# Kernel optimization log

Measured on AMD Instinct MI355X. Metric: run time of the kernel, lower is better.

Reference implementation:

```python
import jax, jax.numpy as jnp
import numpy as np

EPS = 1e-8

def _layernorm(x, gamma, beta):
    # torch-style: std with Bessel correction (ddof=1), eps added to std
    D = x.shape[-1]
    mean = jnp.mean(x, axis=-1, keepdims=True)
    var = jnp.sum((x - mean) ** 2, axis=-1, keepdims=True) / (D - 1)
    std = jnp.sqrt(var)
    return (x - mean) / (std + EPS) * gamma + beta


def setup_inputs() -> dict:
    key = jax.random.key(0)
    B, T, D, H = 1, 2048, 1024, 16
    Dh = D // H
    ks = jax.random.split(key, 8)
    s = 0.02
    return {
        "x": jax.random.normal(ks[0], (B, T, D), jnp.float32),
        "wq": jax.random.normal(ks[1], (H, D, Dh), jnp.float32) * s,
        "wk": jax.random.normal(ks[2], (H, D, Dh), jnp.float32) * s,
        "wv": jax.random.normal(ks[3], (H, D, Dh), jnp.float32) * s,
        "wo": jax.random.normal(ks[4], (D, D), jnp.float32) * s,
        "bo": jnp.zeros((D,), jnp.float32),
        "ln1_g": jnp.ones((D,), jnp.float32),
        "ln1_b": jnp.zeros((D,), jnp.float32),
        "ln2_g": jnp.ones((D,), jnp.float32),
        "ln2_b": jnp.zeros((D,), jnp.float32),
        "w1": jax.random.normal(ks[5], (D, 4 * D), jnp.float32) * s,
        "b1": jnp.zeros((4 * D,), jnp.float32),
        "w2": jax.random.normal(ks[6], (4 * D, D), jnp.float32) * s,
        "b2": jnp.zeros((D,), jnp.float32),
    }


def reference(x, wq, wk, wv, wo, bo, ln1_g, ln1_b, ln2_g, ln2_b, w1, b1, w2, b2):
    B, T, D = x.shape
    H, _, Dh = wq.shape
    # --- attention sublayer (dropout p used at eval => identity) ---
    h = _layernorm(x, ln1_g, ln1_b)
    q = jnp.einsum('btd,hde->bhte', h, wq)
    k = jnp.einsum('btd,hde->bhte', h, wk)
    v = jnp.einsum('btd,hde->bhte', h, wv)
    scores = jnp.einsum('bhte,bhse->bhts', q, k) / jnp.sqrt(jnp.float32(Dh))
    causal = jnp.triu(jnp.ones((T, T), bool), 1)  # True above diagonal => masked
    scores = jnp.where(causal, -jnp.inf, scores)
    attn = jax.nn.softmax(scores, axis=-1)
    ctx = jnp.einsum('bhts,bhse->bthe', attn, v).reshape(B, T, H * Dh)
    att_out = ctx @ wo + bo
    x = x + att_out
    # --- FFN sublayer ---
    h2 = _layernorm(x, ln2_g, ln2_b)
    ffn = jax.nn.gelu(h2 @ w1 + b1, approximate=False) @ w2 + b2
    return x + ffn
```

## Files before the change

kernel.cpp:

```cpp
#include <hip/hip_runtime.h>
#include <hip/hip_bf16.h>
#include <math.h>

typedef unsigned short bf16u;
typedef __attribute__((ext_vector_type(8))) short short8;
typedef __attribute__((ext_vector_type(4))) float floatx4;

__device__ __forceinline__ float bf2f(bf16u u) {
  union { unsigned int i; float f; } c;
  c.i = ((unsigned int)u) << 16;
  return c.f;
}
__device__ __forceinline__ bf16u f2bf(float f) {
  union { float f; unsigned int i; } c;
  c.f = f;
  unsigned int lsb = (c.i >> 16) & 1u;
  c.i += 0x7fffu + lsb;
  return (bf16u)(c.i >> 16);
}

__device__ __forceinline__ void load_lds16(const void* g, void* l) {
  __builtin_amdgcn_global_load_lds(
      (const __attribute__((address_space(1))) void*)g,
      (__attribute__((address_space(3))) void*)l, 16, 0, 0);
}

__global__ __launch_bounds__(256) void ln_kernel(
    const float* __restrict__ x, bf16u* __restrict__ out,
    const float* __restrict__ gamma, const float* __restrict__ beta) {
  const int row = blockIdx.x;
  const int tid = threadIdx.x;
  const int lane = tid & 63, wave = tid >> 6;
  __shared__ float red[4];
  const float* xr = x + (size_t)row * 1024;
  float4 v = ((const float4*)xr)[tid];
  float s = v.x + v.y + v.z + v.w;
#pragma unroll
  for (int off = 32; off; off >>= 1) s += __shfl_down(s, off);
  if (lane == 0) red[wave] = s;
  __syncthreads();
  const float mean = (red[0] + red[1] + red[2] + red[3]) * (1.0f / 1024.0f);
  __syncthreads();
  float d0 = v.x - mean, d1 = v.y - mean, d2 = v.z - mean, d3 = v.w - mean;
  float sq = d0 * d0 + d1 * d1 + d2 * d2 + d3 * d3;
#pragma unroll
  for (int off = 32; off; off >>= 1) sq += __shfl_down(sq, off);
  if (lane == 0) red[wave] = sq;
  __syncthreads();
  const float var = (red[0] + red[1] + red[2] + red[3]) * (1.0f / 1023.0f);
  const float inv = 1.0f / (sqrtf(var) + 1e-8f);
  float4 g = ((const float4*)gamma)[tid];
  float4 b = ((const float4*)beta)[tid];
  uint2 pk;
  pk.x = (unsigned int)f2bf(d0 * inv * g.x + b.x) |
         ((unsigned int)f2bf(d1 * inv * g.y + b.y) << 16);
  pk.y = (unsigned int)f2bf(d2 * inv * g.z + b.z) |
         ((unsigned int)f2bf(d3 * inv * g.w + b.w) << 16);
  *(uint2*)(out + (size_t)row * 1024 + tid * 4) = pk;
}

__global__ __launch_bounds__(256) void pack_weights(
    const float* __restrict__ wq, const float* __restrict__ wk,
    const float* __restrict__ wv, const float* __restrict__ wo,
    const float* __restrict__ w1, const float* __restrict__ w2,
    bf16u* __restrict__ WqkvT, bf16u* __restrict__ woT,
    bf16u* __restrict__ w1T, bf16u* __restrict__ w2T) {
  __shared__ bf16u tile[32][33];
  const int id = blockIdx.x;
  const float* in; bf16u* out; int R, C, bx, by;
  if (id < 3072) {
    int job = id >> 10, rem = id & 1023;
    int head = rem >> 6, t = rem & 63;
    bx = t & 1; by = t >> 1;
    in = (job == 0 ? wq : (job == 1 ? wk : wv)) + head * 65536;
    out = WqkvT + job * 1048576 + head * 65536;
    R = 1024; C = 64;
  } else if (id < 4096) {
    int rem = id - 3072; bx = rem & 31; by = rem >> 5;
    in = wo; out = woT; R = 1024; C = 1024;
  } else if (id < 8192) {
    int rem = id - 4096; bx = rem & 127; by = rem >> 7;
    in = w1; out = w1T; R = 1024; C = 4096;
  } else {
    int rem = id - 8192; bx = rem & 31; by = rem >> 5;
    in = w2; out = w2T; R = 4096; C = 1024;
  }
  const int bc = bx * 32, br = by * 32;
  {
    const int row = threadIdx.x >> 3, c4 = (threadIdx.x & 7) * 4;
    float4 v = *(const float4*)(in + (size_t)(br + row) * C + bc + c4);
    tile[row][c4 + 0] = f2bf(v.x);
    tile[row][c4 + 1] = f2bf(v.y);
    tile[row][c4 + 2] = f2bf(v.z);
    tile[row][c4 + 3] = f2bf(v.w);
  }
  __syncthreads();
  const int lx = threadIdx.x & 31, ly = threadIdx.x >> 5;
#pragma unroll
  for (int i = 0; i < 32; i += 8)
    out[(size_t)(bc + ly + i) * R + br + lx] = tile[lx][ly + i];
}

__global__ __launch_bounds__(256) void transpose_b(
    const bf16u* __restrict__ in, bf16u* __restrict__ out,
    int ins, int coff, int outs) {
  __shared__ bf16u tile[32][33];
  const int bc = blockIdx.x * 32, br = blockIdx.y * 32;
  const int lx = threadIdx.x & 31, ly = threadIdx.x >> 5;
#pragma unroll
  for (int i = 0; i < 32; i += 8)
    tile[ly + i][lx] = in[(size_t)(br + ly + i) * ins + coff + bc + lx];
  __syncthreads();
#pragma unroll
  for (int i = 0; i < 32; i += 8)
    out[(size_t)(bc + ly + i) * outs + br + lx] = tile[lx][ly + i];
}

template <int BM, int BN, int WGR, int WGC, int EPI, int MINW = 4>
__global__ __launch_bounds__(256, MINW) void gemm_bt(
    const bf16u* __restrict__ A, const bf16u* __restrict__ Bt,
    const float* __restrict__ bias, const float* __restrict__ res,
    void* __restrict__ Cout, int M, int N, int K, int kchunk) {
  constexpr int BK = 64;
  constexpr int TM = BM / WGR, TN = BN / WGC;
  constexpr int NI = TM / 16, NJ = TN / 16;
  alignas(16) __shared__ bf16u sA[BM * BK];
  alignas(16) __shared__ bf16u sB[BN * BK];
  const int tid = threadIdx.x, lane = tid & 63, wave = tid >> 6;
  const int wr = wave / WGC, wc = wave % WGC;
  const int quad = lane >> 4, l16 = lane & 15;
  const int m0 = blockIdx.y * BM, n0 = blockIdx.x * BN;
  const int kz = blockIdx.z;
  const int kbeg = kz * kchunk;
  const int kend = (kbeg + kchunk < K) ? (kbeg + kchunk) : K;

  floatx4 acc[NI][NJ] = {};
  constexpr int ACH = BM * BK / 8;
  constexpr int BCH = BN * BK / 8;

  for (int k0 = kbeg; k0 < kend; k0 += BK) {
#pragma unroll
    for (int c = tid; c < ACH; c += 256) {
      int r = c >> 3, kc = ((c ^ r) & 7) * 8;
      load_lds16(A + (size_t)(m0 + r) * K + k0 + kc, (void*)(sA + c * 8));
    }
#pragma unroll
    for (int c = tid; c < BCH; c += 256) {
      int r = c >> 3, kc = ((c ^ r) & 7) * 8;
      load_lds16(Bt + (size_t)(n0 + r) * K + k0 + kc, (void*)(sB + c * 8));
    }
    __syncthreads();
#pragma unroll
    for (int kk = 0; kk < BK; kk += 32) {
      const int ch = (kk >> 3) + quad;
      short8 af[NI], bf[NJ];
#pragma unroll
      for (int i = 0; i < NI; i++) {
        const int R = wr * TM + i * 16 + l16;
        af[i] = *(const short8*)(sA + R * BK + ((ch ^ (R & 7)) << 3));
      }
#pragma unroll
      for (int j = 0; j < NJ; j++) {
        const int R = wc * TN + j * 16 + l16;
        bf[j] = *(const short8*)(sB + R * BK + ((ch ^ (R & 7)) << 3));
      }
#pragma unroll
      for (int i = 0; i < NI; i++)
#pragma unroll
        for (int j = 0; j < NJ; j++)
          acc[i][j] = __builtin_amdgcn_mfma_f32_16x16x32_bf16(af[i], bf[j], acc[i][j], 0, 0, 0);
    }
    __syncthreads();
  }

  float* pout = (float*)Cout;
  if constexpr (EPI == 3) pout += (size_t)kz * M * N;
#pragma unroll
  for (int j = 0; j < NJ; j++) {
    const int col = n0 + wc * TN + j * 16 + l16;
    float bv = 0.0f;
    if constexpr (EPI == 1 || EPI == 2) bv = bias[col];
#pragma unroll
    for (int i = 0; i < NI; i++) {
#pragma unroll
      for (int r = 0; r < 4; r++) {
        const int row = m0 + wr * TM + i * 16 + quad * 4 + r;
        const size_t o = (size_t)row * N + col;
        const float v = acc[i][j][r];
        if constexpr (EPI == 0) {
          ((bf16u*)Cout)[o] = f2bf(v);
        } else if constexpr (EPI == 1) {
          pout[o] = v + bv + res[o];
        } else if constexpr (EPI == 2) {
          float t = v + bv;
          ((bf16u*)Cout)[o] = f2bf(0.5f * t * (1.0f + erff(t * 0.70710678118654752f)));
        } else {
          pout[o] = v;
        }
      }
    }
  }
}

__global__ __launch_bounds__(256) void reduce2_kernel(
    const float* __restrict__ part, const float* __restrict__ bias,
    const float* __restrict__ res, float* __restrict__ out,
    int N, size_t total) {
  size_t i = ((size_t)blockIdx.x * 256 + threadIdx.x) * 4;
  if (i >= total) return;
  float4 a = *(const float4*)(part + i);
  float4 b = *(const float4*)(part + total + i);
  float4 r = *(const float4*)(res + i);
  float4 bv = *(const float4*)(bias + (int)(i & (size_t)(N - 1)));
  float4 o;
  o.x = a.x + b.x + r.x + bv.x;
  o.y = a.y + b.y + r.y + bv.y;
  o.z = a.z + b.z + r.z + bv.z;
  o.w = a.w + b.w + r.w + bv.w;
  *(float4*)(out + i) = o;
}

template <int NZ>
__global__ __launch_bounds__(256, 5) void flash_attn(
    const bf16u* __restrict__ QKV, const bf16u* __restrict__ Vt,
    bf16u* __restrict__ partO, float* __restrict__ partL) {
  const int qb = 31 - blockIdx.x;
  const int h = blockIdx.y;
  const int z = blockIdx.z;
  const int tid = threadIdx.x, lane = tid & 63, wave = tid >> 6;
  const int quad = lane >> 4, l16 = lane & 15;
  alignas(16) __shared__ bf16u sQ[64 * 64];
  alignas(16) __shared__ bf16u sK[64 * 64];
  alignas(16) __shared__ bf16u sVt[64 * 64];
  alignas(16) __shared__ bf16u sP[64 * 64];
  const int q0 = qb * 64;
  const int nkt = qb + 1;
  const int rq = wave * 16 + l16;

#pragma unroll
  for (int c = tid; c < 512; c += 256) {
    int r = c >> 3, kc = (c ^ r) & 7;
    load_lds16(QKV + (size_t)(q0 + r) * 3072 + h * 64 + kc * 8, (void*)(sQ + c * 8));
  }
  int kt = z;
  if (kt < nkt) {
    const int c0 = kt * 64;
#pragma unroll
    for (int c = tid; c < 512; c += 256) {
      int r = c >> 3, kc = (c ^ r) & 7;
      load_lds16(QKV + (size_t)(c0 + r) * 3072 + 1024 + h * 64 + kc * 8, (void*)(sK + c * 8));
    }
#pragma unroll
    for (int c = tid; c < 512; c += 256) {
      int e = c >> 3, kc = (c ^ e) & 7;
      load_lds16(Vt + (size_t)(h * 64 + e) * 2048 + c0 + kc * 8, (void*)(sVt + c * 8));
    }
  }
  __syncthreads();

  floatx4 acc_l = {0.f, 0.f, 0.f, 0.f};
  floatx4 aco[4] = {};
  short8 ones;
#pragma unroll
  for (int u = 0; u < 8; u++) ones[u] = (short)0x3F80;

  for (; kt < nkt; kt += NZ) {
    const int c0 = kt * 64;
    floatx4 s[4] = {};
    __builtin_amdgcn_s_setprio(1);
#pragma unroll
    for (int kk = 0; kk < 64; kk += 32) {
      const int ch = (kk >> 3) + quad;
      short8 aq = *(const short8*)(sQ + rq * 64 + ((ch ^ (rq & 7)) << 3));
#pragma unroll
      for (int nt = 0; nt < 4; nt++) {
        const int rk = nt * 16 + l16;
        short8 bk = *(const short8*)(sK + rk * 64 + ((ch ^ (rk & 7)) << 3));
        s[nt] = __builtin_amdgcn_mfma_f32_16x16x32_bf16(bk, aq, s[nt], 0, 0, 0);
      }
    }
    __builtin_amdgcn_s_setprio(0);
    const float C = 0.125f * 1.44269504088896f;
    const bool diag = (kt == qb);
#pragma unroll
    for (int nt = 0; nt < 4; nt++)
#pragma unroll
      for (int r = 0; r < 4; r++) {
        float t = s[nt][r] * C;
        if (diag) {
          const int kpos = c0 + nt * 16 + quad * 4 + r;
          if (kpos > q0 + rq) t = -__builtin_inff();
        }
        s[nt][r] = __builtin_amdgcn_exp2f(t);
      }
#pragma unroll
    for (int nt = 0; nt < 4; nt++) {
      unsigned int lo = (unsigned int)f2bf(s[nt][0]) | ((unsigned int)f2bf(s[nt][1]) << 16);
      unsigned int hi = (unsigned int)f2bf(s[nt][2]) | ((unsigned int)f2bf(s[nt][3]) << 16);
      uint2 pk; pk.x = lo; pk.y = hi;
      const int e0 = nt * 16 + quad * 4;
      const int cch = e0 >> 3, sub = e0 & 7;
      *(uint2*)(sP + rq * 64 + ((cch ^ (rq & 7)) << 3) + sub) = pk;
    }
    __syncthreads();
    if (kt + NZ < nkt) {
      const int c0n = (kt + NZ) * 64;
#pragma unroll
      for (int c = tid; c < 512; c += 256) {
        int r = c >> 3, kc = (c ^ r) & 7;
        load_lds16(QKV + (size_t)(c0n + r) * 3072 + 1024 + h * 64 + kc * 8,
                   (void*)(sK + c * 8));
      }
    }
    __builtin_amdgcn_s_setprio(1);
#pragma unroll
    for (int kk = 0; kk < 64; kk += 32) {
      const int ch = (kk >> 3) + quad;
      short8 ap = *(const short8*)(sP + rq * 64 + ((ch ^ (rq & 7)) << 3));
#pragma unroll
      for (int dt = 0; dt < 4; dt++) {
        const int rv = dt * 16 + l16;
        short8 bv = *(const short8*)(sVt + rv * 64 + ((ch ^ (rv & 7)) << 3));
        aco[dt] = __builtin_amdgcn_mfma_f32_16x16x32_bf16(ap, bv, aco[dt], 0, 0, 0);
      }
      acc_l = __builtin_amdgcn_mfma_f32_16x16x32_bf16(ap, ones, acc_l, 0, 0, 0);
    }
    __builtin_amdgcn_s_setprio(0);
    __syncthreads();
    if (kt + NZ < nkt) {
      const int c0n = (kt + NZ) * 64;
#pragma unroll
      for (int c = tid; c < 512; c += 256) {
        int e = c >> 3, kc = (c ^ e) & 7;
        load_lds16(Vt + (size_t)(h * 64 + e) * 2048 + c0n + kc * 8,
                   (void*)(sVt + c * 8));
      }
    }
  }

  bf16u* po = partO + ((size_t)z * 2048 + q0) * 1024 + h * 64;
#pragma unroll
  for (int dt = 0; dt < 4; dt++)
#pragma unroll
    for (int r = 0; r < 4; r++)
      po[(wave * 16 + quad * 4 + r) * 1024 + dt * 16 + l16] = f2bf(aco[dt][r]);
  if (l16 == 0) {
#pragma unroll
    for (int r = 0; r < 4; r++)
      partL[((size_t)z * 2048 + q0 + wave * 16 + quad * 4 + r) * 16 + h] = acc_l[r];
  }
}

template <int NZ>
__global__ __launch_bounds__(256) void attn_reduce(
    const bf16u* __restrict__ partO, const float* __restrict__ partL,
    bf16u* __restrict__ ctx) {
  const int t = blockIdx.x;
  const int col = threadIdx.x * 4;
  const int h = col >> 6;
  float l = 0.f;
#pragma unroll
  for (int z = 0; z < NZ; z++) l += partL[((size_t)z * 2048 + t) * 16 + h];
  float o0 = 0.f, o1 = 0.f, o2 = 0.f, o3 = 0.f;
#pragma unroll
  for (int z = 0; z < NZ; z++) {
    uint2 v = *(const uint2*)(partO + ((size_t)z * 2048 + t) * 1024 + col);
    o0 += bf2f((bf16u)(v.x & 0xffff)); o1 += bf2f((bf16u)(v.x >> 16));
    o2 += bf2f((bf16u)(v.y & 0xffff)); o3 += bf2f((bf16u)(v.y >> 16));
  }
  const float inv = 1.0f / l;
  uint2 pk;
  pk.x = (unsigned int)f2bf(o0 * inv) | ((unsigned int)f2bf(o1 * inv) << 16);
  pk.y = (unsigned int)f2bf(o2 * inv) | ((unsigned int)f2bf(o3 * inv) << 16);
  *(uint2*)(ctx + (size_t)t * 1024 + col) = pk;
}

extern "C" void kernel_launch(void* const* d_in, const int* in_sizes, int n_in,
                              void* d_out, int out_size, void* d_ws, size_t ws_size,
                              hipStream_t stream) {
  (void)in_sizes; (void)n_in; (void)out_size; (void)ws_size;
  const float* x   = (const float*)d_in[0];
  const float* wq  = (const float*)d_in[1];
  const float* wk  = (const float*)d_in[2];
  const float* wv  = (const float*)d_in[3];
  const float* wo  = (const float*)d_in[4];
  const float* bo  = (const float*)d_in[5];
  const float* g1  = (const float*)d_in[6];
  const float* be1 = (const float*)d_in[7];
  const float* g2  = (const float*)d_in[8];
  const float* be2 = (const float*)d_in[9];
  const float* w1  = (const float*)d_in[10];
  const float* bb1 = (const float*)d_in[11];
  const float* w2  = (const float*)d_in[12];
  const float* bb2 = (const float*)d_in[13];

  char* p = (char*)d_ws;
  const size_t MB = 1024 * 1024;
  constexpr int NZ = 4;
  bf16u* WqkvT = (bf16u*)(p + 0 * MB);
  bf16u* woT   = (bf16u*)(p + 6 * MB);
  bf16u* w1T   = (bf16u*)(p + 8 * MB);
  bf16u* w2T   = (bf16u*)(p + 16 * MB);
  bf16u* multi = (bf16u*)(p + 24 * MB);
  bf16u* QKV   = (bf16u*)(p + 28 * MB);
  float* partL = (float*)(p + 40 * MB);
  bf16u* partO = (bf16u*)(p + 41 * MB);
  bf16u* mid   = (bf16u*)(p + 28 * MB);
  float* x1    = (float*)(p + 49 * MB);
  float* partF = (float*)(p + 0 * MB);
  bf16u* hln = multi, *Vtr = multi, *ctx = multi, *h2 = multi;

  pack_weights<<<12288, 256, 0, stream>>>(wq, wk, wv, wo, w1, w2,
                                          WqkvT, woT, w1T, w2T);

  ln_kernel<<<2048, 256, 0, stream>>>(x, hln, g1, be1);
  gemm_bt<64, 64, 2, 2, 0, 6><<<dim3(48, 32, 1), 256, 0, stream>>>(
      hln, WqkvT, nullptr, nullptr, QKV, 2048, 3072, 1024, 1024);
  transpose_b<<<dim3(32, 64), 256, 0, stream>>>(QKV, Vtr, 3072, 2048, 2048);
  flash_attn<NZ><<<dim3(32, 16, NZ), 256, 0, stream>>>(QKV, Vtr, partO, partL);
  attn_reduce<NZ><<<2048, 256, 0, stream>>>(partO, partL, ctx);
  gemm_bt<32, 64, 2, 2, 1, 6><<<dim3(16, 64, 1), 256, 0, stream>>>(
      ctx, woT, bo, x, x1, 2048, 1024, 1024, 1024);
  ln_kernel<<<2048, 256, 0, stream>>>(x1, h2, g2, be2);
  gemm_bt<64, 64, 2, 2, 2, 6><<<dim3(64, 32, 1), 256, 0, stream>>>(
      h2, w1T, bb1, nullptr, mid, 2048, 4096, 1024, 1024);
  gemm_bt<64, 64, 2, 2, 3, 6><<<dim3(16, 32, 2), 256, 0, stream>>>(
      mid, w2T, nullptr, nullptr, partF, 2048, 1024, 4096, 2048);
  reduce2_kernel<<<2048, 256, 0, stream>>>(partF, bb2, x1, (float*)d_out,
                                           1024, (size_t)2048 * 1024);
}
```

Measured before the change: 268.7 us.

## Fuse LN1 into weight pack, V transpose into QKV epilogue, attn reduce into Wo GEMM

Adds the first layernorm as extra blocks of the weight-packing kernel. The QKV GEMM epilogue now writes V columns transposed directly, which removes the separate transpose kernel. The attention split-K combine (sum of partials and divide by l) moves into the A-tile load of the output-projection GEMM, removing the attn_reduce kernel and the ctx round trip. Together these cut three launches and intermediate traffic, but the Wo GEMM A-load now goes through registers instead of direct-to-LDS and recomputes the reduction once per N-tile, and its tile changes from 32x64 to 64x64.

```diff
diff --git a/kernel.cpp b/kernel.cpp
--- a/kernel.cpp
+++ b/kernel.cpp
@@ -25,14 +25,11 @@
       (__attribute__((address_space(3))) void*)l, 16, 0, 0);
 }
 
-__global__ __launch_bounds__(256) void ln_kernel(
-    const float* __restrict__ x, bf16u* __restrict__ out,
-    const float* __restrict__ gamma, const float* __restrict__ beta) {
-  const int row = blockIdx.x;
-  const int tid = threadIdx.x;
+__device__ __forceinline__ void ln_row(
+    const float* __restrict__ xr, bf16u* __restrict__ orow,
+    const float* __restrict__ gamma, const float* __restrict__ beta,
+    float* red, int tid) {
   const int lane = tid & 63, wave = tid >> 6;
-  __shared__ float red[4];
-  const float* xr = x + (size_t)row * 1024;
   float4 v = ((const float4*)xr)[tid];
   float s = v.x + v.y + v.z + v.w;
 #pragma unroll
@@ -56,17 +53,35 @@
          ((unsigned int)f2bf(d1 * inv * g.y + b.y) << 16);
   pk.y = (unsigned int)f2bf(d2 * inv * g.z + b.z) |
          ((unsigned int)f2bf(d3 * inv * g.w + b.w) << 16);
-  *(uint2*)(out + (size_t)row * 1024 + tid * 4) = pk;
-}
-
-__global__ __launch_bounds__(256) void pack_weights(
+  *(uint2*)(orow + tid * 4) = pk;
+}
+
+__global__ __launch_bounds__(256) void ln_kernel(
+    const float* __restrict__ x, bf16u* __restrict__ out,
+    const float* __restrict__ gamma, const float* __restrict__ beta) {
+  __shared__ float red[4];
+  const int row = blockIdx.x;
+  ln_row(x + (size_t)row * 1024, out + (size_t)row * 1024, gamma, beta, red,
+         threadIdx.x);
+}
+
+__global__ __launch_bounds__(256) void pack_ln(
     const float* __restrict__ wq, const float* __restrict__ wk,
     const float* __restrict__ wv, const float* __restrict__ wo,
     const float* __restrict__ w1, const float* __restrict__ w2,
     bf16u* __restrict__ WqkvT, bf16u* __restrict__ woT,
-    bf16u* __restrict__ w1T, bf16u* __restrict__ w2T) {
+    bf16u* __restrict__ w1T, bf16u* __restrict__ w2T,
+    const float* __restrict__ x, bf16u* __restrict__ hln,
+    const float* __restrict__ g1, const float* __restrict__ be1) {
   __shared__ bf16u tile[32][33];
+  __shared__ float red[4];
   const int id = blockIdx.x;
+  if (id >= 12288) {
+    const int row = id - 12288;
+    ln_row(x + (size_t)row * 1024, hln + (size_t)row * 1024, g1, be1, red,
+           threadIdx.x);
+    return;
+  }
   const float* in; bf16u* out; int R, C, bx, by;
   if (id < 3072) {
     int job = id >> 10, rem = id & 1023;
@@ -101,26 +116,12 @@
     out[(size_t)(bc + ly + i) * R + br + lx] = tile[lx][ly + i];
 }
 
-__global__ __launch_bounds__(256) void transpose_b(
-    const bf16u* __restrict__ in, bf16u* __restrict__ out,
-    int ins, int coff, int outs) {
-  __shared__ bf16u tile[32][33];
-  const int bc = blockIdx.x * 32, br = blockIdx.y * 32;
-  const int lx = threadIdx.x & 31, ly = threadIdx.x >> 5;
-#pragma unroll
-  for (int i = 0; i < 32; i += 8)
-    tile[ly + i][lx] = in[(size_t)(br + ly + i) * ins + coff + bc + lx];
-  __syncthreads();
-#pragma unroll
-  for (int i = 0; i < 32; i += 8)
-    out[(size_t)(bc + ly + i) * outs + br + lx] = tile[lx][ly + i];
-}
-
-template <int BM, int BN, int WGR, int WGC, int EPI, int MINW = 4>
+template <int BM, int BN, int WGR, int WGC, int EPI, int MINW = 4, int ASRC = 0>
 __global__ __launch_bounds__(256, MINW) void gemm_bt(
     const bf16u* __restrict__ A, const bf16u* __restrict__ Bt,
     const float* __restrict__ bias, const float* __restrict__ res,
-    void* __restrict__ Cout, int M, int N, int K, int kchunk) {
+    void* __restrict__ Cout, int M, int N, int K, int kchunk,
+    const float* __restrict__ aux) {
   constexpr int BK = 64;
   constexpr int TM = BM / WGR, TN = BN / WGC;
   constexpr int NI = TM / 16, NJ = TN / 16;
@@ -142,7 +143,31 @@
 #pragma unroll
     for (int c = tid; c < ACH; c += 256) {
       int r = c >> 3, kc = ((c ^ r) & 7) * 8;
-      load_lds16(A + (size_t)(m0 + r) * K + k0 + kc, (void*)(sA + c * 8));
+      if constexpr (ASRC == 0) {
+        load_lds16(A + (size_t)(m0 + r) * K + k0 + kc, (void*)(sA + c * 8));
+      } else {
+        const int t = m0 + r;
+        const int f0 = k0 + kc;
+        const int hh = f0 >> 6;
+        float l = 0.f;
+        float o0 = 0, o1 = 0, o2 = 0, o3 = 0, o4 = 0, o5 = 0, o6 = 0, o7 = 0;
+#pragma unroll
+        for (int z = 0; z < 4; z++) {
+          l += aux[((size_t)z * 2048 + t) * 16 + hh];
+          uint4 v = *(const uint4*)(A + ((size_t)z * 2048 + t) * 1024 + f0);
+          o0 += bf2f((bf16u)(v.x & 0xffff)); o1 += bf2f((bf16u)(v.x >> 16));
+          o2 += bf2f((bf16u)(v.y & 0xffff)); o3 += bf2f((bf16u)(v.y >> 16));
+          o4 += bf2f((bf16u)(v.z & 0xffff)); o5 += bf2f((bf16u)(v.z >> 16));
+          o6 += bf2f((bf16u)(v.w & 0xffff)); o7 += bf2f((bf16u)(v.w >> 16));
+        }
+        const float inv = 1.0f / l;
+        uint4 pk;
+        pk.x = (unsigned int)f2bf(o0 * inv) | ((unsigned int)f2bf(o1 * inv) << 16);
+        pk.y = (unsigned int)f2bf(o2 * inv) | ((unsigned int)f2bf(o3 * inv) << 16);
+        pk.z = (unsigned int)f2bf(o4 * inv) | ((unsigned int)f2bf(o5 * inv) << 16);
+        pk.w = (unsigned int)f2bf(o6 * inv) | ((unsigned int)f2bf(o7 * inv) << 16);
+        *(uint4*)(sA + c * 8) = pk;
+      }
     }
 #pragma unroll
     for (int c = tid; c < BCH; c += 256) {
@@ -182,20 +207,36 @@
     if constexpr (EPI == 1 || EPI == 2) bv = bias[col];
 #pragma unroll
     for (int i = 0; i < NI; i++) {
-#pragma unroll
-      for (int r = 0; r < 4; r++) {
-        const int row = m0 + wr * TM + i * 16 + quad * 4 + r;
-        const size_t o = (size_t)row * N + col;
-        const float v = acc[i][j][r];
-        if constexpr (EPI == 0) {
-          ((bf16u*)Cout)[o] = f2bf(v);
-        } else if constexpr (EPI == 1) {
-          pout[o] = v + bv + res[o];
-        } else if constexpr (EPI == 2) {
-          float t = v + bv;
-          ((bf16u*)Cout)[o] = f2bf(0.5f * t * (1.0f + erff(t * 0.70710678118654752f)));
+      if constexpr (EPI == 4) {
+        const int row0 = m0 + wr * TM + i * 16 + quad * 4;
+        if (col < 2048) {
+#pragma unroll
+          for (int r = 0; r < 4; r++)
+            ((bf16u*)Cout)[(size_t)(row0 + r) * N + col] = f2bf(acc[i][j][r]);
         } else {
-          pout[o] = v;
+          uint2 pk;
+          pk.x = (unsigned int)f2bf(acc[i][j][0]) |
+                 ((unsigned int)f2bf(acc[i][j][1]) << 16);
+          pk.y = (unsigned int)f2bf(acc[i][j][2]) |
+                 ((unsigned int)f2bf(acc[i][j][3]) << 16);
+          *(uint2*)((bf16u*)res + (size_t)(col - 2048) * 2048 + row0) = pk;
+        }
+      } else {
+#pragma unroll
+        for (int r = 0; r < 4; r++) {
+          const int row = m0 + wr * TM + i * 16 + quad * 4 + r;
+          const size_t o = (size_t)row * N + col;
+          const float v = acc[i][j][r];
+          if constexpr (EPI == 0) {
+            ((bf16u*)Cout)[o] = f2bf(v);
+          } else if constexpr (EPI == 1) {
+            pout[o] = v + bv + res[o];
+          } else if constexpr (EPI == 2) {
+            float t = v + bv;
+            ((bf16u*)Cout)[o] = f2bf(0.5f * t * (1.0f + erff(t * 0.70710678118654752f)));
+          } else if constexpr (EPI == 3) {
+            pout[o] = v;
+          }
         }
       }
     }
@@ -349,30 +390,6 @@
     for (int r = 0; r < 4; r++)
       partL[((size_t)z * 2048 + q0 + wave * 16 + quad * 4 + r) * 16 + h] = acc_l[r];
   }
-}
-
-template <int NZ>
-__global__ __launch_bounds__(256) void attn_reduce(
-    const bf16u* __restrict__ partO, const float* __restrict__ partL,
-    bf16u* __restrict__ ctx) {
-  const int t = blockIdx.x;
-  const int col = threadIdx.x * 4;
-  const int h = col >> 6;
-  float l = 0.f;
-#pragma unroll
-  for (int z = 0; z < NZ; z++) l += partL[((size_t)z * 2048 + t) * 16 + h];
-  float o0 = 0.f, o1 = 0.f, o2 = 0.f, o3 = 0.f;
-#pragma unroll
-  for (int z = 0; z < NZ; z++) {
-    uint2 v = *(const uint2*)(partO + ((size_t)z * 2048 + t) * 1024 + col);
-    o0 += bf2f((bf16u)(v.x & 0xffff)); o1 += bf2f((bf16u)(v.x >> 16));
-    o2 += bf2f((bf16u)(v.y & 0xffff)); o3 += bf2f((bf16u)(v.y >> 16));
-  }
-  const float inv = 1.0f / l;
-  uint2 pk;
-  pk.x = (unsigned int)f2bf(o0 * inv) | ((unsigned int)f2bf(o1 * inv) << 16);
-  pk.y = (unsigned int)f2bf(o2 * inv) | ((unsigned int)f2bf(o3 * inv) << 16);
-  *(uint2*)(ctx + (size_t)t * 1024 + col) = pk;
 }
 
 extern "C" void kernel_launch(void* const* d_in, const int* in_sizes, int n_in,
@@ -405,27 +422,25 @@
   bf16u* QKV   = (bf16u*)(p + 28 * MB);
   float* partL = (float*)(p + 40 * MB);
   bf16u* partO = (bf16u*)(p + 41 * MB);
+  float* x1    = (float*)(p + 57 * MB);
+  bf16u* Vtr   = (bf16u*)(p + 65 * MB);
   bf16u* mid   = (bf16u*)(p + 28 * MB);
-  float* x1    = (float*)(p + 49 * MB);
   float* partF = (float*)(p + 0 * MB);
-  bf16u* hln = multi, *Vtr = multi, *ctx = multi, *h2 = multi;
-
-  pack_weights<<<12288, 256, 0, stream>>>(wq, wk, wv, wo, w1, w2,
-                                          WqkvT, woT, w1T, w2T);
-
-  ln_kernel<<<2048, 256, 0, stream>>>(x, hln, g1, be1);
-  gemm_bt<64, 64, 2, 2, 0, 6><<<dim3(48, 32, 1), 256, 0, stream>>>(
-      hln, WqkvT, nullptr, nullptr, QKV, 2048, 3072, 1024, 1024);
-  transpose_b<<<dim3(32, 64), 256, 0, stream>>>(QKV, Vtr, 3072, 2048, 2048);
+  bf16u* hln = multi, *h2 = multi;
+
+  pack_ln<<<14336, 256, 0, stream>>>(wq, wk, wv, wo, w1, w2,
+                                     WqkvT, woT, w1T, w2T, x, hln, g1, be1);
+  gemm_bt<64, 64, 2, 2, 4, 6><<<dim3(48, 32, 1), 256, 0, stream>>>(
+      hln, WqkvT, nullptr, (const float*)Vtr, QKV, 2048, 3072, 1024, 1024,
+      nullptr);
   flash_attn<NZ><<<dim3(32, 16, NZ), 256, 0, stream>>>(QKV, Vtr, partO, partL);
-  attn_reduce<NZ><<<2048, 256, 0, stream>>>(partO, partL, ctx);
-  gemm_bt<32, 64, 2, 2, 1, 6><<<dim3(16, 64, 1), 256, 0, stream>>>(
-      ctx, woT, bo, x, x1, 2048, 1024, 1024, 1024);
+  gemm_bt<64, 64, 2, 2, 1, 6, 1><<<dim3(16, 32, 1), 256, 0, stream>>>(
+      partO, woT, bo, x, x1, 2048, 1024, 1024, 1024, partL);
   ln_kernel<<<2048, 256, 0, stream>>>(x1, h2, g2, be2);
   gemm_bt<64, 64, 2, 2, 2, 6><<<dim3(64, 32, 1), 256, 0, stream>>>(
-      h2, w1T, bb1, nullptr, mid, 2048, 4096, 1024, 1024);
+      h2, w1T, bb1, nullptr, mid, 2048, 4096, 1024, 1024, nullptr);
   gemm_bt<64, 64, 2, 2, 3, 6><<<dim3(16, 32, 2), 256, 0, stream>>>(
-      mid, w2T, nullptr, nullptr, partF, 2048, 1024, 4096, 2048);
+      mid, w2T, nullptr, nullptr, partF, 2048, 1024, 4096, 2048, nullptr);
   reduce2_kernel<<<2048, 256, 0, stream>>>(partF, bb2, x1, (float*)d_out,
                                            1024, (size_t)2048 * 1024);
 }
```

Measured after the change: 310.2 us. +15.5%, slower.
